# Kernel optimization log

Hardware: AMD Instinct MI355X
Metric: run time of the kernel (lower is better)

## Reference

```python
import math
import jax, jax.numpy as jnp
import numpy as np

DEPTH, EMB, HEADS = 6, 768, 12
B, N = 2, 2048
LN_EPS = 1e-6


def _get_attention_slopes(n):
    def p2(n):
        start = 2 ** (-2 ** (-(math.log2(n) - 3)))
        return [start * start ** i for i in range(n)]
    if math.log2(n).is_integer():
        return p2(n)
    c = 2 ** math.floor(math.log2(n))
    return p2(c) + _get_attention_slopes(2 * c)[0::2][: n - c]


def layer_norm(x, scale, bias):
    m = jnp.mean(x, axis=-1, keepdims=True)
    v = jnp.var(x, axis=-1, keepdims=True)
    return (x - m) * jax.lax.rsqrt(v + LN_EPS) * scale + bias


def setup_inputs() -> dict:
    key = jax.random.key(0)
    ks = jax.random.split(key, 6)
    s = 0.02
    return {
        "x": jax.random.normal(ks[0], (B, N, EMB), jnp.float32),
        "wqkv": jax.random.normal(ks[1], (DEPTH, EMB, 3 * EMB), jnp.float32) * s,
        "bqkv": jnp.zeros((DEPTH, 3 * EMB), jnp.float32),
        "wo": jax.random.normal(ks[2], (DEPTH, EMB, EMB), jnp.float32) * s,
        "bo": jnp.zeros((DEPTH, EMB), jnp.float32),
        "ln1s": jnp.ones((DEPTH, EMB), jnp.float32),
        "ln1b": jnp.zeros((DEPTH, EMB), jnp.float32),
        "ln2s": jnp.ones((DEPTH, EMB), jnp.float32),
        "ln2b": jnp.zeros((DEPTH, EMB), jnp.float32),
        "w1": jax.random.normal(ks[3], (DEPTH, EMB, 4 * EMB), jnp.float32) * s,
        "w2": jax.random.normal(ks[4], (DEPTH, 4 * EMB, EMB), jnp.float32) * s,
        "lnfs": jnp.ones((EMB,), jnp.float32),
        "lnfb": jnp.zeros((EMB,), jnp.float32),
    }


def reference(x, wqkv, bqkv, wo, bo, ln1s, ln1b, ln2s, ln2b, w1, w2, lnfs, lnfb):
    Bx, n, E = x.shape
    H = HEADS
    Dh = E // H
    scale = Dh ** -0.5
    slopes = jnp.asarray(_get_attention_slopes(H), dtype=x.dtype)  # [H]
    # ALiBi-style bias: slope[h] * key-position (absolute), per source code
    pos_bias = slopes[:, None, None] * jnp.arange(n, dtype=x.dtype)[None, None, :]  # [H,1,n]
    causal = jnp.tril(jnp.ones((n, n), bool))
    big_neg = jnp.finfo(x.dtype).min

    def block(h, p):
        Wqkv, Bqkv, Wo, Bo, L1s, L1b, L2s, L2b, W1, W2 = p
        y = layer_norm(h, L1s, L1b)
        qkv = y @ Wqkv + Bqkv  # [B,n,3E]
        q, k, v = jnp.split(qkv, 3, axis=-1)
        mh = lambda t: t.reshape(Bx, n, H, Dh).transpose(0, 2, 1, 3)  # b h n d
        q, k, v = mh(q), mh(k), mh(v)
        att = jnp.einsum("bhnd,bhmd->bhnm", q, k) * scale + pos_bias[None]
        att = jnp.where(causal, att, big_neg)
        att = jax.nn.softmax(att, axis=-1)
        o = jnp.einsum("bhnm,bhmd->bhnd", att, v)
        o = o.transpose(0, 2, 1, 3).reshape(Bx, n, E) @ Wo + Bo
        h = h + o
        y = layer_norm(h, L2s, L2b)
        y = jax.nn.gelu(y @ W1) @ W2  # fc1 (no bias) -> gelu -> fc2 (no bias)
        return h + y, None

    h, _ = jax.lax.scan(block, x, (wqkv, bqkv, wo, bo, ln1s, ln1b, ln2s, ln2b, w1, w2))
    return layer_norm(h, lnfs, lnfb)
```

## Files before the change

kernel.cpp:

```cpp
#include <hip/hip_runtime.h>
#include <hip/hip_bf16.h>
#include <stdint.h>


typedef __bf16 bf16_t;
typedef __bf16 bf16x8 __attribute__((ext_vector_type(8)));
typedef __bf16 bf16x4 __attribute__((ext_vector_type(4)));
typedef float f32x4 __attribute__((ext_vector_type(4)));

#define EMB   768
#define NSEQ  2048
#define BATCH 2
#define NHEAD 12
#define NDEPTH 6
#define MROWS (BATCH * NSEQ)

__constant__ float c_slopes[NHEAD] = {
    0.5f, 0.25f, 0.125f, 0.0625f, 0.03125f, 0.015625f, 0.0078125f, 0.00390625f,
    0.7071067811865476f, 0.3535533905932738f, 0.1767766952966369f, 0.08838834764831845f};

__device__ __forceinline__ void gld_lds16(const void* g, void* l) {
  __builtin_amdgcn_global_load_lds(
      (const __attribute__((address_space(1))) uint32_t*)g,
      (__attribute__((address_space(3))) uint32_t*)l, 16, 0, 0);
}

__global__ void detect_kernel(const void* __restrict__ lnfs, int* __restrict__ flag) {
  if (threadIdx.x == 0 && blockIdx.x == 0) {
    uint32_t u = *(const uint32_t*)lnfs;
    *flag = (u == 0x3F800000u) ? 0 : 1;
  }
}

__global__ void fill_one_kernel(bf16_t* __restrict__ o, int n) {
  int i = blockIdx.x * blockDim.x + threadIdx.x;
  if (i < n) o[i] = (bf16_t)1.0f;
}

__global__ void cast_kernel(const void* __restrict__ x_, float* __restrict__ h, int n,
                            const int* __restrict__ flagp) {
  const int flag = *flagp;
  int i = blockIdx.x * blockDim.x + threadIdx.x;
  if (i < n) h[i] = flag ? (float)((const bf16_t*)x_)[i] : ((const float*)x_)[i];
}

template <int FINAL>
__global__ __launch_bounds__(256) void ln_kernel(const float* __restrict__ x,
                                                 const void* __restrict__ sc_,
                                                 const void* __restrict__ bi_,
                                                 size_t eoff, void* __restrict__ y_,
                                                 const int* __restrict__ flagp) {
  const int flag = *flagp;
  const int widx = blockIdx.x * 4 + (threadIdx.x >> 6);
  const int lane = threadIdx.x & 63;
  const float* row = x + (size_t)widx * EMB;
  float v[12];
  float sum = 0.f, ss = 0.f;
#pragma unroll
  for (int i = 0; i < 12; ++i) {
    float t = row[lane + i * 64];
    v[i] = t; sum += t; ss += t * t;
  }
#pragma unroll
  for (int m = 1; m < 64; m <<= 1) {
    sum += __shfl_xor(sum, m, 64);
    ss  += __shfl_xor(ss, m, 64);
  }
  const float mean = sum * (1.f / 768.f);
  const float var  = ss * (1.f / 768.f) - mean * mean;
  const float rs   = rsqrtf(var + 1e-6f);
#pragma unroll
  for (int i = 0; i < 12; ++i) {
    const int d = lane + i * 64;
    const float s = flag ? (float)((const bf16_t*)sc_)[eoff + d] : ((const float*)sc_)[eoff + d];
    const float b = flag ? (float)((const bf16_t*)bi_)[eoff + d] : ((const float*)bi_)[eoff + d];
    const float o = (v[i] - mean) * rs * s + b;
    if (FINAL == 0 || flag) ((bf16_t*)y_)[(size_t)widx * EMB + d] = (bf16_t)o;
    else                    ((float*)y_)[(size_t)widx * EMB + d] = o;
  }
}

__global__ __launch_bounds__(256) void transpose_k(const void* __restrict__ W_, size_t eoff,
                                                   bf16_t* __restrict__ T, int R, int C,
                                                   const int* __restrict__ flagp) {
  __shared__ bf16_t tile[64][72];
  const int c0 = blockIdx.x * 64, r0 = blockIdx.y * 64;
  const int t = threadIdx.x;
  if (*flagp) {
    const bf16_t* W = (const bf16_t*)W_ + eoff;
#pragma unroll
    for (int k = 0; k < 2; ++k) {
      int idx = t + k * 256;
      int r = idx >> 3, s = idx & 7;
      *(bf16x8*)&tile[r][s * 8] = *(const bf16x8*)(W + (size_t)(r0 + r) * C + c0 + s * 8);
    }
  } else {
    const float* W = (const float*)W_ + eoff;
#pragma unroll
    for (int q = 0; q < 16; ++q) {
      int idx = t + q * 256;
      int r = idx >> 6, c = idx & 63;
      tile[r][c] = (bf16_t)W[(size_t)(r0 + r) * C + c0 + c];
    }
  }
  __syncthreads();
#pragma unroll
  for (int k = 0; k < 2; ++k) {
    int idx = t + k * 256;
    int orow = idx >> 3, s = idx & 7;
    bf16x8 v;
#pragma unroll
    for (int q = 0; q < 8; ++q) v[q] = tile[s * 8 + q][orow];
    *(bf16x8*)(T + (size_t)(c0 + orow) * R + r0 + s * 8) = v;
  }
}

__device__ __forceinline__ float gelu_f(float x) {
  float u = 0.7978845608028654f * (x + 0.044715f * x * x * x);
  float t = tanhf(u);
  return 0.5f * x * (1.0f + t);
}

template <int MODE>
__global__ __launch_bounds__(256) void gemm_bt(const bf16_t* __restrict__ A,
                                               const bf16_t* __restrict__ Bt,
                                               const void* __restrict__ bias_, size_t boff,
                                               bf16_t* __restrict__ out,
                                               float* __restrict__ hio, int N, int K,
                                               const int* __restrict__ flagp) {
  __shared__ bf16_t Als[128 * 32];
  __shared__ bf16_t Bls[128 * 32];
  const int flag = *flagp;
  const int tid = threadIdx.x;
  const int wave = tid >> 6, lane = tid & 63;
  const int bm = blockIdx.y * 128, bn = blockIdx.x * 128;
  const int kc = blockIdx.z;
  const int Kc = K / (int)gridDim.z;
  const int kbeg = kc * Kc, kend = kbeg + Kc;
  const int wm = (wave >> 1) * 64, wn = (wave & 1) * 64;
  const int rl = lane & 15, quad = lane >> 4;

  f32x4 acc[4][4];
#pragma unroll
  for (int i = 0; i < 4; ++i)
#pragma unroll
    for (int j = 0; j < 4; ++j) acc[i][j] = (f32x4){0.f, 0.f, 0.f, 0.f};

  const int tr0 = wave * 32 + (lane >> 2);
  const int tc  = (lane & 3) * 8;

  for (int k0 = kbeg; k0 < kend; k0 += 32) {
#pragma unroll
    for (int j = 0; j < 2; ++j) {
      const int tr = tr0 + j * 16;
      gld_lds16(A  + (size_t)(bm + tr) * K + k0 + tc, &Als[tr * 32 + tc]);
      gld_lds16(Bt + (size_t)(bn + tr) * K + k0 + tc, &Bls[tr * 32 + tc]);
    }
    __syncthreads();
    bf16x8 af[4], bfv[4];
#pragma unroll
    for (int i = 0; i < 4; ++i) af[i] = *(const bf16x8*)&Als[(wm + i * 16 + rl) * 32 + quad * 8];
#pragma unroll
    for (int j = 0; j < 4; ++j) bfv[j] = *(const bf16x8*)&Bls[(wn + j * 16 + rl) * 32 + quad * 8];
#pragma unroll
    for (int i = 0; i < 4; ++i)
#pragma unroll
      for (int j = 0; j < 4; ++j)
        acc[i][j] = __builtin_amdgcn_mfma_f32_16x16x32_bf16(af[i], bfv[j], acc[i][j], 0, 0, 0);
    __syncthreads();
  }

  const int r0 = bm + wm + quad * 4;
  const int cb = bn + wn + rl;
#pragma unroll
  for (int j = 0; j < 4; ++j) {
    const int c = cb + j * 16;
    const float bv = (bias_ && kc == 0)
                         ? (flag ? (float)((const bf16_t*)bias_)[boff + c]
                                 : ((const float*)bias_)[boff + c])
                         : 0.f;
#pragma unroll
    for (int i = 0; i < 4; ++i) {
      const int rbase = r0 + i * 16;
      f32x4 a = acc[i][j];
#pragma unroll
      for (int rr = 0; rr < 4; ++rr) {
        const float v = a[rr] + bv;
        const size_t idx = (size_t)(rbase + rr) * N + c;
        if (MODE == 0) out[idx] = (bf16_t)v;
        else if (MODE == 1) out[idx] = (bf16_t)gelu_f(v);
        else atomicAdd(&hio[idx], v);
      }
    }
  }
}

__global__ __launch_bounds__(256) void gemm_qkv(const bf16_t* __restrict__ A,
                                                const bf16_t* __restrict__ Bt,
                                                const void* __restrict__ bias_, size_t boff,
                                                bf16_t* __restrict__ Qb,
                                                bf16_t* __restrict__ Kpk,
                                                bf16_t* __restrict__ Vtp,
                                                const int* __restrict__ flagp) {
  constexpr int N = 3 * EMB, K = EMB;
  __shared__ bf16_t Als[128 * 32];
  __shared__ bf16_t Bls[128 * 32];
  const int flag = *flagp;
  const int tid = threadIdx.x;
  const int wave = tid >> 6, lane = tid & 63;
  const int bm = blockIdx.y * 128, bn = blockIdx.x * 128;
  const int wm = (wave >> 1) * 64, wn = (wave & 1) * 64;
  const int rl = lane & 15, quad = lane >> 4;

  f32x4 acc[4][4];
#pragma unroll
  for (int i = 0; i < 4; ++i)
#pragma unroll
    for (int j = 0; j < 4; ++j) acc[i][j] = (f32x4){0.f, 0.f, 0.f, 0.f};

  const int tr0 = wave * 32 + (lane >> 2);
  const int tc  = (lane & 3) * 8;

  for (int k0 = 0; k0 < K; k0 += 32) {
#pragma unroll
    for (int j = 0; j < 2; ++j) {
      const int tr = tr0 + j * 16;
      gld_lds16(A  + (size_t)(bm + tr) * K + k0 + tc, &Als[tr * 32 + tc]);
      gld_lds16(Bt + (size_t)(bn + tr) * K + k0 + tc, &Bls[tr * 32 + tc]);
    }
    __syncthreads();
    bf16x8 af[4], bfv[4];
#pragma unroll
    for (int i = 0; i < 4; ++i) af[i] = *(const bf16x8*)&Als[(wm + i * 16 + rl) * 32 + quad * 8];
#pragma unroll
    for (int j = 0; j < 4; ++j) bfv[j] = *(const bf16x8*)&Bls[(wn + j * 16 + rl) * 32 + quad * 8];
#pragma unroll
    for (int i = 0; i < 4; ++i)
#pragma unroll
      for (int j = 0; j < 4; ++j)
        acc[i][j] = __builtin_amdgcn_mfma_f32_16x16x32_bf16(af[i], bfv[j], acc[i][j], 0, 0, 0);
    __syncthreads();
  }

  const int r0 = bm + wm + quad * 4;
  const int cb = bn + wn + rl;
  const int seg = bn / EMB;
#pragma unroll
  for (int j = 0; j < 4; ++j) {
    const int c = cb + j * 16;
    const float bv = flag ? (float)((const bf16_t*)bias_)[boff + c]
                          : ((const float*)bias_)[boff + c];
    const int cc = c - seg * EMB;
    const int hh = cc >> 6, d = cc & 63;
#pragma unroll
    for (int i = 0; i < 4; ++i) {
      const int rbase = r0 + i * 16;
      const int bb = rbase >> 11, n0 = rbase & 2047;
      f32x4 a = acc[i][j];
      if (seg == 0) {
#pragma unroll
        for (int rr = 0; rr < 4; ++rr)
          Qb[(size_t)(rbase + rr) * EMB + cc] = (bf16_t)(a[rr] + bv);
      } else if (seg == 1) {
        const size_t kidx = ((size_t)(bb * NHEAD + hh) * NSEQ + n0) * 64 + d;
#pragma unroll
        for (int rr = 0; rr < 4; ++rr)
          Kpk[kidx + (size_t)rr * 64] = (bf16_t)(a[rr] + bv);
      } else {
        bf16x4 pk;
#pragma unroll
        for (int rr = 0; rr < 4; ++rr) pk[rr] = (bf16_t)(a[rr] + bv);
        *(bf16x4*)&Vtp[((size_t)(bb * NHEAD + hh) * 64 + d) * NSEQ + n0] = pk;
      }
    }
  }
}

__global__ __launch_bounds__(256) void attn_flash(const bf16_t* __restrict__ Qb,
                                                  const bf16_t* __restrict__ Kpk,
                                                  const bf16_t* __restrict__ Vtp,
                                                  bf16_t* __restrict__ o) {
  __shared__ bf16_t Kls[2][64][72];
  __shared__ bf16_t Vls[2][64][72];
  __shared__ bf16_t Pls[4][16][72];
  const int tid = threadIdx.x;
  const int wave = tid >> 6, lane = tid & 63;
  const int qt = 31 - (int)blockIdx.x;
  const int bh = blockIdx.y;
  const int h = bh % NHEAD, b = bh / NHEAD;
  const float slope = c_slopes[h];
  const int q0 = qt * 64 + wave * 16;
  const int rl = lane & 15, quad = lane >> 4;

  const bf16_t* qbase = Qb + (size_t)(b * NSEQ + q0 + rl) * EMB + h * 64;
  const bf16x8 qf0 = *(const bf16x8*)(qbase + quad * 8);
  const bf16x8 qf1 = *(const bf16x8*)(qbase + 32 + quad * 8);

  const bf16_t* kg = Kpk + (size_t)bh * NSEQ * 64;
  const bf16_t* vg = Vtp + (size_t)bh * 64 * NSEQ;

  f32x4 acc[4];
#pragma unroll
  for (int db = 0; db < 4; ++db) acc[db] = (f32x4){0.f, 0.f, 0.f, 0.f};
  float lsum = 0.f;

  const int skey = tid >> 2, sc = (tid & 3) * 16;
  const int vdim = tid >> 2, vk = (tid & 3) * 16;
  const int vswz = (vdim >> 3) & 3;
  const int vo0 = (((vk >> 3) + 0) ^ vswz) * 8;
  const int vo1 = (((vk >> 3) + 1) ^ vswz) * 8;

  const float mq = slope * (float)(q0 + rl);
  float aoff[4][4];
#pragma unroll
  for (int f = 0; f < 4; ++f)
#pragma unroll
    for (int r = 0; r < 4; ++r)
      aoff[f][r] = slope * (float)(f * 16 + quad * 4 + r) - mq;

  const int pswz = (rl >> 2) & 3;
  int pbase[4];
#pragma unroll
  for (int f = 0; f < 4; ++f) {
    const int oct = f * 2 + (quad >> 1);
    const int osw = (oct & 4) | ((oct & 3) ^ pswz);
    pbase[f] = osw * 8 + (quad & 1) * 4;
  }

  const int ntiles = qt + 1;
  bf16x8 kr0, kr1, vr0, vr1;
  {
    const bf16_t* kp_ = kg + (size_t)skey * 64 + sc;
    kr0 = *(const bf16x8*)kp_;
    kr1 = *(const bf16x8*)(kp_ + 8);
    const bf16_t* vp_ = vg + (size_t)vdim * NSEQ + vk;
    vr0 = *(const bf16x8*)vp_;
    vr1 = *(const bf16x8*)(vp_ + 8);
  }

  for (int t = 0; t < ntiles; ++t) {
    const int p = t & 1;
    const int kb = t * 64;
    *(bf16x8*)&Kls[p][skey][sc]     = kr0;
    *(bf16x8*)&Kls[p][skey][sc + 8] = kr1;
    *(bf16x8*)&Vls[p][vdim][vo0]    = vr0;
    *(bf16x8*)&Vls[p][vdim][vo1]    = vr1;
    __syncthreads();
    if (t + 1 < ntiles) {
      const bf16_t* kp_ = kg + (size_t)(kb + 64 + skey) * 64 + sc;
      kr0 = *(const bf16x8*)kp_;
      kr1 = *(const bf16x8*)(kp_ + 8);
      const bf16_t* vp_ = vg + (size_t)vdim * NSEQ + kb + 64 + vk;
      vr0 = *(const bf16x8*)vp_;
      vr1 = *(const bf16x8*)(vp_ + 8);
    }

    f32x4 s2[4];
#pragma unroll
    for (int f = 0; f < 4; ++f) {
      const bf16x8 kf0 = *(const bf16x8*)&Kls[p][f * 16 + rl][quad * 8];
      const bf16x8 kf1 = *(const bf16x8*)&Kls[p][f * 16 + rl][32 + quad * 8];
      f32x4 z = (f32x4){0.f, 0.f, 0.f, 0.f};
      z = __builtin_amdgcn_mfma_f32_16x16x32_bf16(kf0, qf0, z, 0, 0, 0);
      z = __builtin_amdgcn_mfma_f32_16x16x32_bf16(kf1, qf1, z, 0, 0, 0);
      s2[f] = z;
    }

    const bool full = (kb + 63 <= q0);
    const float kbase = slope * (float)kb;
#pragma unroll
    for (int f = 0; f < 4; ++f) {
      bf16x4 pk;
#pragma unroll
      for (int r = 0; r < 4; ++r) {
        const int key = kb + f * 16 + quad * 4 + r;
        const bool valid = full || (key <= q0 + rl);
        const float e = valid ? __expf(fmaf(s2[f][r], 0.125f, kbase + aoff[f][r])) : 0.f;
        lsum += e;
        pk[r] = (bf16_t)e;
      }
      *(bf16x4*)&Pls[wave][rl][pbase[f]] = pk;
    }

    const bf16x8 pf0 = *(const bf16x8*)&Pls[wave][rl][(quad ^ pswz) * 8];
    const bf16x8 pf1 = *(const bf16x8*)&Pls[wave][rl][32 + (quad ^ pswz) * 8];
#pragma unroll
    for (int db = 0; db < 4; ++db) {
      const int dim = db * 16 + rl;
      const int vs = (dim >> 3) & 3;
      const bf16x8 vf0 = *(const bf16x8*)&Vls[p][dim][(quad ^ vs) * 8];
      const bf16x8 vf1 = *(const bf16x8*)&Vls[p][dim][(4 + (quad ^ vs)) * 8];
      acc[db] = __builtin_amdgcn_mfma_f32_16x16x32_bf16(pf0, vf0, acc[db], 0, 0, 0);
      acc[db] = __builtin_amdgcn_mfma_f32_16x16x32_bf16(pf1, vf1, acc[db], 0, 0, 0);
    }
  }

  float lt = lsum;
  lt += __shfl_xor(lt, 16, 64);
  lt += __shfl_xor(lt, 32, 64);
#pragma unroll
  for (int r = 0; r < 4; ++r) {
    const float linv = 1.f / __shfl(lt, quad * 4 + r, 64);
    const size_t rowo = (size_t)(b * NSEQ + q0 + quad * 4 + r) * EMB + h * 64;
#pragma unroll
    for (int db = 0; db < 4; ++db)
      o[rowo + db * 16 + rl] = (bf16_t)(acc[db][r] * linv);
  }
}

extern "C" void kernel_launch(void* const* d_in, const int* in_sizes, int n_in,
                              void* d_out, int out_size, void* d_ws, size_t ws_size,
                              hipStream_t stream) {
  const void* x    = d_in[0];
  const void* wqkv = d_in[1];
  const void* bqkv = d_in[2];
  const void* wo   = d_in[3];
  const void* bo   = d_in[4];
  const void* ln1s = d_in[5];
  const void* ln1b = d_in[6];
  const void* ln2s = d_in[7];
  const void* ln2b = d_in[8];
  const void* w1   = d_in[9];
  const void* w2   = d_in[10];
  const void* lnfs = d_in[11];
  const void* lnfb = d_in[12];

  const size_t need = 12582912ull + 6291456ull + 25165824ull + 4718592ull + 256ull;
  if (ws_size < need) {
    fill_one_kernel<<<(out_size + 255) / 256, 256, 0, stream>>>((bf16_t*)d_out, out_size);
    return;
  }

  char* p = (char*)d_ws;
  float*  h  = (float*)p;  p += 12582912ull;
  bf16_t* y  = (bf16_t*)p; p += 6291456ull;
  bf16_t* u  = (bf16_t*)p; p += 25165824ull;
  bf16_t* wT = (bf16_t*)p; p += 4718592ull;
  int* flagp = (int*)p;
  bf16_t* Qb   = u;
  bf16_t* Kpk  = u + 3145728;
  bf16_t* Vtp  = u + 6291456;
  bf16_t* t1   = u;
  bf16_t* attno = y;

  detect_kernel<<<1, 64, 0, stream>>>(lnfs, flagp);
  cast_kernel<<<(MROWS * EMB) / 256, 256, 0, stream>>>(x, h, MROWS * EMB, flagp);

  for (int l = 0; l < NDEPTH; ++l) {
    const size_t sE   = (size_t)l * EMB;
    const size_t s3E  = (size_t)l * 3 * EMB;
    const size_t wq_o = (size_t)l * EMB * 3 * EMB;
    const size_t wo_o = (size_t)l * EMB * EMB;
    const size_t w1_o = (size_t)l * EMB * 4 * EMB;

    ln_kernel<0><<<MROWS / 4, 256, 0, stream>>>(h, ln1s, ln1b, sE, y, flagp);
    transpose_k<<<dim3(36, 12), 256, 0, stream>>>(wqkv, wq_o, wT, 768, 2304, flagp);
    gemm_qkv<<<dim3(18, 32), 256, 0, stream>>>(y, wT, bqkv, s3E, Qb, Kpk, Vtp, flagp);
    attn_flash<<<dim3(32, BATCH * NHEAD), 256, 0, stream>>>(Qb, Kpk, Vtp, attno);
    transpose_k<<<dim3(12, 12), 256, 0, stream>>>(wo, wo_o, wT, 768, 768, flagp);
    gemm_bt<2><<<dim3(6, 32, 4), 256, 0, stream>>>(attno, wT, bo, sE, nullptr, h,
                                                   EMB, EMB, flagp);
    ln_kernel<0><<<MROWS / 4, 256, 0, stream>>>(h, ln2s, ln2b, sE, y, flagp);
    transpose_k<<<dim3(48, 12), 256, 0, stream>>>(w1, w1_o, wT, 768, 3072, flagp);
    gemm_bt<1><<<dim3(24, 32), 256, 0, stream>>>(y, wT, nullptr, 0, t1, nullptr,
                                                 4 * EMB, EMB, flagp);
    transpose_k<<<dim3(12, 48), 256, 0, stream>>>(w2, w1_o, wT, 3072, 768, flagp);
    gemm_bt<2><<<dim3(6, 32, 4), 256, 0, stream>>>(t1, wT, nullptr, 0, nullptr, h,
                                                   EMB, 4 * EMB, flagp);
  }
  ln_kernel<1><<<MROWS / 4, 256, 0, stream>>>(h, lnfs, lnfb, 0, d_out, flagp);
}
```

Before: 1.788 ms.

## Double-buffer GEMM LDS tiles and remap blocks across XCDs

Both GEMM kernels now use two LDS buffers and prefetch the next K-tile with global_load_lds while MFMAs run on the current one, synchronising with explicit vmcnt waits and raw barriers. Launches become 1D grids whose block index is remapped so consecutive tiles land on the same XCD (blockIdx & 7 chunking), aiming at better L2 reuse. The goal is to hide global load latency and cut cache misses. In exchange it doubles LDS use, which may lower occupancy, and it relies on the 4-loads-per-stage vmcnt accounting being correct.

Result: no change. 1.765 ms (-1.3%).

```diff
diff --git a/kernel.cpp b/kernel.cpp
--- a/kernel.cpp
+++ b/kernel.cpp
@@ -127,16 +127,21 @@
                                                const void* __restrict__ bias_, size_t boff,
                                                bf16_t* __restrict__ out,
                                                float* __restrict__ hio, int N, int K,
+                                               int nbn, int nkc,
                                                const int* __restrict__ flagp) {
-  __shared__ bf16_t Als[128 * 32];
-  __shared__ bf16_t Bls[128 * 32];
+  __shared__ bf16_t Als[2][128 * 32];
+  __shared__ bf16_t Bls[2][128 * 32];
   const int flag = *flagp;
   const int tid = threadIdx.x;
   const int wave = tid >> 6, lane = tid & 63;
-  const int bm = blockIdx.y * 128, bn = blockIdx.x * 128;
-  const int kc = blockIdx.z;
-  const int Kc = K / (int)gridDim.z;
-  const int kbeg = kc * Kc, kend = kbeg + Kc;
+  const int per = (int)gridDim.x >> 3;
+  const int lin = ((int)blockIdx.x & 7) * per + ((int)blockIdx.x >> 3);
+  const int bn = (lin % nbn) * 128;
+  const int bm = ((lin / nbn) & 31) * 128;
+  const int kc = lin / (nbn * 32);
+  const int Kc = K / nkc;
+  const int kbeg = kc * Kc;
+  const int nkt = Kc / 32;
   const int wm = (wave >> 1) * 64, wn = (wave & 1) * 64;
   const int rl = lane & 15, quad = lane >> 4;
 
@@ -149,25 +154,36 @@
   const int tr0 = wave * 32 + (lane >> 2);
   const int tc  = (lane & 3) * 8;
 
-  for (int k0 = kbeg; k0 < kend; k0 += 32) {
+  auto STAGE = [&](int p, int k0) {
 #pragma unroll
     for (int j = 0; j < 2; ++j) {
       const int tr = tr0 + j * 16;
-      gld_lds16(A  + (size_t)(bm + tr) * K + k0 + tc, &Als[tr * 32 + tc]);
-      gld_lds16(Bt + (size_t)(bn + tr) * K + k0 + tc, &Bls[tr * 32 + tc]);
-    }
-    __syncthreads();
+      gld_lds16(A  + (size_t)(bm + tr) * K + k0 + tc, &Als[p][tr * 32 + tc]);
+      gld_lds16(Bt + (size_t)(bn + tr) * K + k0 + tc, &Bls[p][tr * 32 + tc]);
+    }
+  };
+
+  STAGE(0, kbeg);
+  for (int it = 0; it < nkt; ++it) {
+    const int p = it & 1;
+    if (it + 1 < nkt) {
+      STAGE(p ^ 1, kbeg + (it + 1) * 32);
+      asm volatile("s_waitcnt vmcnt(4)" ::: "memory");
+    } else {
+      asm volatile("s_waitcnt vmcnt(0)" ::: "memory");
+    }
+    __builtin_amdgcn_s_barrier();
     bf16x8 af[4], bfv[4];
 #pragma unroll
-    for (int i = 0; i < 4; ++i) af[i] = *(const bf16x8*)&Als[(wm + i * 16 + rl) * 32 + quad * 8];
-#pragma unroll
-    for (int j = 0; j < 4; ++j) bfv[j] = *(const bf16x8*)&Bls[(wn + j * 16 + rl) * 32 + quad * 8];
+    for (int i = 0; i < 4; ++i) af[i] = *(const bf16x8*)&Als[p][(wm + i * 16 + rl) * 32 + quad * 8];
+#pragma unroll
+    for (int j = 0; j < 4; ++j) bfv[j] = *(const bf16x8*)&Bls[p][(wn + j * 16 + rl) * 32 + quad * 8];
 #pragma unroll
     for (int i = 0; i < 4; ++i)
 #pragma unroll
       for (int j = 0; j < 4; ++j)
         acc[i][j] = __builtin_amdgcn_mfma_f32_16x16x32_bf16(af[i], bfv[j], acc[i][j], 0, 0, 0);
-    __syncthreads();
+    __builtin_amdgcn_s_barrier();
   }
 
   const int r0 = bm + wm + quad * 4;
@@ -203,12 +219,16 @@
                                                 bf16_t* __restrict__ Vtp,
                                                 const int* __restrict__ flagp) {
   constexpr int N = 3 * EMB, K = EMB;
-  __shared__ bf16_t Als[128 * 32];
-  __shared__ bf16_t Bls[128 * 32];
+  constexpr int nbn = 18;
+  __shared__ bf16_t Als[2][128 * 32];
+  __shared__ bf16_t Bls[2][128 * 32];
   const int flag = *flagp;
   const int tid = threadIdx.x;
   const int wave = tid >> 6, lane = tid & 63;
-  const int bm = blockIdx.y * 128, bn = blockIdx.x * 128;
+  const int per = (int)gridDim.x >> 3;
+  const int lin = ((int)blockIdx.x & 7) * per + ((int)blockIdx.x >> 3);
+  const int bn = (lin % nbn) * 128;
+  const int bm = (lin / nbn) * 128;
   const int wm = (wave >> 1) * 64, wn = (wave & 1) * 64;
   const int rl = lane & 15, quad = lane >> 4;
 
@@ -221,25 +241,37 @@
   const int tr0 = wave * 32 + (lane >> 2);
   const int tc  = (lane & 3) * 8;
 
-  for (int k0 = 0; k0 < K; k0 += 32) {
+  auto STAGE = [&](int p, int k0) {
 #pragma unroll
     for (int j = 0; j < 2; ++j) {
       const int tr = tr0 + j * 16;
-      gld_lds16(A  + (size_t)(bm + tr) * K + k0 + tc, &Als[tr * 32 + tc]);
-      gld_lds16(Bt + (size_t)(bn + tr) * K + k0 + tc, &Bls[tr * 32 + tc]);
-    }
-    __syncthreads();
+      gld_lds16(A  + (size_t)(bm + tr) * K + k0 + tc, &Als[p][tr * 32 + tc]);
+      gld_lds16(Bt + (size_t)(bn + tr) * K + k0 + tc, &Bls[p][tr * 32 + tc]);
+    }
+  };
+
+  constexpr int nkt = K / 32;
+  STAGE(0, 0);
+  for (int it = 0; it < nkt; ++it) {
+    const int p = it & 1;
+    if (it + 1 < nkt) {
+      STAGE(p ^ 1, (it + 1) * 32);
+      asm volatile("s_waitcnt vmcnt(4)" ::: "memory");
+    } else {
+      asm volatile("s_waitcnt vmcnt(0)" ::: "memory");
+    }
+    __builtin_amdgcn_s_barrier();
     bf16x8 af[4], bfv[4];
 #pragma unroll
-    for (int i = 0; i < 4; ++i) af[i] = *(const bf16x8*)&Als[(wm + i * 16 + rl) * 32 + quad * 8];
-#pragma unroll
-    for (int j = 0; j < 4; ++j) bfv[j] = *(const bf16x8*)&Bls[(wn + j * 16 + rl) * 32 + quad * 8];
+    for (int i = 0; i < 4; ++i) af[i] = *(const bf16x8*)&Als[p][(wm + i * 16 + rl) * 32 + quad * 8];
+#pragma unroll
+    for (int j = 0; j < 4; ++j) bfv[j] = *(const bf16x8*)&Bls[p][(wn + j * 16 + rl) * 32 + quad * 8];
 #pragma unroll
     for (int i = 0; i < 4; ++i)
 #pragma unroll
       for (int j = 0; j < 4; ++j)
         acc[i][j] = __builtin_amdgcn_mfma_f32_16x16x32_bf16(af[i], bfv[j], acc[i][j], 0, 0, 0);
-    __syncthreads();
+    __builtin_amdgcn_s_barrier();
   }
 
   const int r0 = bm + wm + quad * 4;
@@ -455,18 +487,18 @@
 
     ln_kernel<0><<<MROWS / 4, 256, 0, stream>>>(h, ln1s, ln1b, sE, y, flagp);
     transpose_k<<<dim3(36, 12), 256, 0, stream>>>(wqkv, wq_o, wT, 768, 2304, flagp);
-    gemm_qkv<<<dim3(18, 32), 256, 0, stream>>>(y, wT, bqkv, s3E, Qb, Kpk, Vtp, flagp);
+    gemm_qkv<<<18 * 32, 256, 0, stream>>>(y, wT, bqkv, s3E, Qb, Kpk, Vtp, flagp);
     attn_flash<<<dim3(32, BATCH * NHEAD), 256, 0, stream>>>(Qb, Kpk, Vtp, attno);
     transpose_k<<<dim3(12, 12), 256, 0, stream>>>(wo, wo_o, wT, 768, 768, flagp);
-    gemm_bt<2><<<dim3(6, 32, 4), 256, 0, stream>>>(attno, wT, bo, sE, nullptr, h,
-                                                   EMB, EMB, flagp);
+    gemm_bt<2><<<6 * 32 * 4, 256, 0, stream>>>(attno, wT, bo, sE, nullptr, h,
+                                               EMB, EMB, 6, 4, flagp);
     ln_kernel<0><<<MROWS / 4, 256, 0, stream>>>(h, ln2s, ln2b, sE, y, flagp);
     transpose_k<<<dim3(48, 12), 256, 0, stream>>>(w1, w1_o, wT, 768, 3072, flagp);
-    gemm_bt<1><<<dim3(24, 32), 256, 0, stream>>>(y, wT, nullptr, 0, t1, nullptr,
-                                                 4 * EMB, EMB, flagp);
+    gemm_bt<1><<<24 * 32, 256, 0, stream>>>(y, wT, nullptr, 0, t1, nullptr,
+                                            4 * EMB, EMB, 24, 1, flagp);
     transpose_k<<<dim3(12, 48), 256, 0, stream>>>(w2, w1_o, wT, 3072, 768, flagp);
-    gemm_bt<2><<<dim3(6, 32, 4), 256, 0, stream>>>(t1, wT, nullptr, 0, nullptr, h,
-                                                   EMB, 4 * EMB, flagp);
+    gemm_bt<2><<<6 * 32 * 4, 256, 0, stream>>>(t1, wT, nullptr, 0, nullptr, h,
+                                               EMB, 4 * EMB, 6, 4, flagp);
   }
   ln_kernel<1><<<MROWS / 4, 256, 0, stream>>>(h, lnfs, lnfb, 0, d_out, flagp);
 }
```
